# Performance work log

Hardware: AMD Instinct MI355X
Metric: run time of the kernel (lower is better)

Reference implementation:

```python
import jax, jax.numpy as jnp
import numpy as np

B, C, H, W = 64, 2048, 14, 14
D, S, ITERS, EPS, HID = 256, 8, 3, 1e-8, 512


def build_pos(h, w, d):
    gy, gx = np.meshgrid(np.arange(h), np.arange(w), indexing='ij')
    q = d // 4
    omega = 1.0 / (10000.0 ** (np.arange(q) / q))
    ey = gy.reshape(-1, 1) * omega
    ex = gx.reshape(-1, 1) * omega
    pe = np.concatenate([np.sin(ey), np.cos(ey), np.sin(ex), np.cos(ex)], axis=1)
    return jnp.asarray(pe[None], jnp.float32)  # (1, h*w, d)


def layernorm(x, g, b, eps=1e-5):
    m = x.mean(-1, keepdims=True)
    v = ((x - m) ** 2).mean(-1, keepdims=True)
    return (x - m) * jax.lax.rsqrt(v + eps) * g + b


def setup_inputs() -> dict:
    key = jax.random.key(0)
    ks = jax.random.split(key, 16)
    w = lambda k, shp, s=0.02: jax.random.normal(k, shp, jnp.float32) * s
    inp = {
        'x': jax.random.normal(ks[0], (B, C, H, W), jnp.float32),
        'slot_noise': jax.random.normal(ks[1], (B, S, D), jnp.float32),
        'conv_w': w(ks[2], (C, D)), 'conv_b': jnp.zeros((D,), jnp.float32),
        'pos': build_pos(H, W, D),
        'slots_mu': jax.random.normal(ks[3], (1, 1, D), jnp.float32),
        'slots_logsigma': -jnp.ones((1, 1, D), jnp.float32),
        'qw': w(ks[4], (D, D)), 'qb': jnp.zeros((D,), jnp.float32),
        'kw': w(ks[5], (D, D)), 'kb': jnp.zeros((D,), jnp.float32),
        'vw': w(ks[6], (D, D)), 'vb': jnp.zeros((D,), jnp.float32),
        'gru_wih': w(ks[7], (D, 3 * D)), 'gru_whh': w(ks[8], (D, 3 * D)),
        'gru_bih': jnp.zeros((3 * D,), jnp.float32), 'gru_bhh': jnp.zeros((3 * D,), jnp.float32),
        'w1': w(ks[9], (D, HID)), 'b1': jnp.zeros((HID,), jnp.float32),
        'w2': w(ks[10], (HID, D)), 'b2': jnp.zeros((D,), jnp.float32),
        'ln_in_g': jnp.ones((D,), jnp.float32), 'ln_in_b': jnp.zeros((D,), jnp.float32),
        'ln_s_g': jnp.ones((D,), jnp.float32), 'ln_s_b': jnp.zeros((D,), jnp.float32),
        'ln_ff_g': jnp.ones((D,), jnp.float32), 'ln_ff_b': jnp.zeros((D,), jnp.float32),
    }
    return inp


def reference(x, slot_noise, conv_w, conv_b, pos, slots_mu, slots_logsigma,
              qw, qb, kw, kb, vw, vb, gru_wih, gru_whh, gru_bih, gru_bhh,
              w1, b1, w2, b2, ln_in_g, ln_in_b, ln_s_g, ln_s_b, ln_ff_g, ln_ff_b):
    b, c, h, w_ = x.shape
    d = qw.shape[0]
    scale = d ** (-0.5)
    # (B,C,H,W) -> (B,N,C) -> project -> add pos
    xt = x.transpose(0, 2, 3, 1).reshape(b, h * w_, c)
    xt = xt @ conv_w + conv_b + pos
    # slot init
    slots = slots_mu + jnp.exp(slots_logsigma) * slot_noise  # (B,S,D)
    inp = layernorm(xt, ln_in_g, ln_in_b)
    k = inp @ kw + kb
    v = inp @ vw + vb
    attn = None
    for _ in range(ITERS):
        slots_prev = slots
        s = layernorm(slots, ln_s_g, ln_s_b)
        q = s @ qw + qb
        dots = jnp.einsum('bid,bjd->bij', q, k) * scale  # (B,S,N)
        attn = jax.nn.softmax(dots, axis=1) + EPS  # softmax over slots
        attn = attn / attn.sum(-1, keepdims=True)  # renormalize over keys
        updates = jnp.einsum('bjd,bij->bid', v, attn)  # (B,S,D)
        # GRUCell (torch semantics)
        gi = updates @ gru_wih + gru_bih
        gh = slots_prev @ gru_whh + gru_bhh
        ir, iz, inn = jnp.split(gi, 3, axis=-1)
        hr, hz, hn = jnp.split(gh, 3, axis=-1)
        r = jax.nn.sigmoid(ir + hr)
        z = jax.nn.sigmoid(iz + hz)
        nn_ = jnp.tanh(inn + r * hn)
        slots = (1.0 - z) * nn_ + z * slots_prev
        ff = layernorm(slots, ln_ff_g, ln_ff_b)
        slots = slots + (jax.nn.relu(ff @ w1 + b1)) @ w2 + b2
    attn_map = attn.reshape(b, S, h, w_)
    return slots, attn_map
```

## Files before the change

kernel.cpp:

```cpp
#include <hip/hip_runtime.h>
#include <stdint.h>

#define HWN 196
#define CIN 2048
#define DD  256
#define BB  64
#define NSLOT 8
#define KVPAD 224
#define MTOT 12544
#define PPB 208

typedef __attribute__((ext_vector_type(8))) short short8;
typedef __attribute__((ext_vector_type(4))) float f32x4;
typedef __attribute__((ext_vector_type(4))) unsigned short us4;

__device__ __forceinline__ ushort f2bf(float f){ union{float f;uint32_t u;}v;v.f=f;uint32_t u=v.u;return (ushort)((u+0x7FFFu+((u>>16)&1u))>>16);}
__device__ __forceinline__ float bf2f(ushort h){ union{uint32_t u;float f;}v;v.u=((uint32_t)h)<<16;return v.f;}
__device__ __forceinline__ float sigm(float x){ return 1.f/(1.f+expf(-x)); }

__device__ __forceinline__ short8 ldsY(const ushort* buf, int LD, int kt, int lane){
    int row = lane & 15;
    int ch = kt*4 + (lane>>4);
    return *(const short8*)&buf[row*LD + ((ch ^ (row&7))<<3)];
}
__device__ __forceinline__ short8 gX(const ushort* base, int K, int nrow, int kt, int lane){
    return *(const short8*)&base[(size_t)nrow*K + kt*32 + (lane>>4)*8];
}

struct TD { const float* s; ushort* d; int R, C, t0; };
struct TD8 { TD a[8]; };

__global__ __launch_bounds__(256) void k_prep(TD8 td){
    __shared__ float tile[32][33];
    int bt = blockIdx.x;
    int mi = 0;
    #pragma unroll
    for (int i = 1; i < 8; ++i) if (bt >= td.a[i].t0) mi = i;
    TD d = td.a[mi];
    int lt = bt - d.t0;
    int tilesx = (d.C + 31) >> 5;
    int cb = (lt % tilesx) * 32, rb = (lt / tilesx) * 32;
    int tx = threadIdx.x & 31, ty = threadIdx.x >> 5;
    for (int i = ty; i < 32; i += 8) {
        int r = rb + i, c = cb + tx;
        tile[i][tx] = (r < d.R && c < d.C) ? d.s[(size_t)r * d.C + c] : 0.f;
    }
    __syncthreads();
    for (int i = ty; i < 32; i += 8) {
        int c = cb + i, r = rb + tx;
        if (c < d.C && r < d.R) d.d[(size_t)c * d.R + r] = f2bf(tile[tx][i]);
    }
}

__global__ __launch_bounds__(512) void k_proj(const float* __restrict__ x,
        const ushort* __restrict__ cwT, float* __restrict__ Cpart){
    __shared__ ushort As[2][PPB*72];
    const int t = threadIdx.x, lane = t & 63, wv = t >> 6;
    const int bid = blockIdx.x;
    const int b = bid >> 2, nh = (bid >> 1) & 1, kq = bid & 1;
    const int gn = nh*128 + wv*16 + (lane&15);
    const float* xb = x + (size_t)b*(CIN*HWN) + (size_t)(kq*1024)*HWN;
    const ushort* cw = cwT + (size_t)gn*CIN + kq*1024 + (lane>>4)*8;

    f32x4 acc[13] = {};
    f32x4 sreg[7];

    {
        const f32x4* xs = (const f32x4*)xb;
        #pragma unroll
        for (int i = 0; i < 7; ++i){ int idx = t + i*512; if (idx < 3136) sreg[i] = xs[idx]; }
        #pragma unroll
        for (int i = 0; i < 7; ++i){
            int idx = t + i*512;
            if (idx < 3136){
                int c = idx/49, p = (idx - c*49)*4;
                #pragma unroll
                for (int j = 0; j < 4; ++j) As[0][(p+j)*72 + c] = f2bf(sreg[i][j]);
            }
        }
    }
    __syncthreads();
    int cur = 0;
    for (int s = 0; s < 16; ++s){
        if (s < 15){
            const f32x4* xs = (const f32x4*)(xb + (size_t)(s+1)*64*HWN);
            #pragma unroll
            for (int i = 0; i < 7; ++i){ int idx = t + i*512; if (idx < 3136) sreg[i] = xs[idx]; }
        }
        #pragma unroll
        for (int kk = 0; kk < 2; ++kk){
            short8 bf = *(const short8*)&cw[s*64 + kk*32];
            short8 afr[13];
            #pragma unroll
            for (int mi = 0; mi < 13; ++mi)
                afr[mi] = *(const short8*)&As[cur][(mi*16 + (lane&15))*72 + (kk*4 + (lane>>4))*8];
            #pragma unroll
            for (int mi = 0; mi < 13; ++mi)
                acc[mi] = __builtin_amdgcn_mfma_f32_16x16x32_bf16(afr[mi], bf, acc[mi], 0,0,0);
        }
        if (s < 15){
            #pragma unroll
            for (int i = 0; i < 7; ++i){
                int idx = t + i*512;
                if (idx < 3136){
                    int c = idx/49, p = (idx - c*49)*4;
                    #pragma unroll
                    for (int j = 0; j < 4; ++j) As[cur^1][(p+j)*72 + c] = f2bf(sreg[i][j]);
                }
            }
        }
        __syncthreads();
        cur ^= 1;
    }
    float* outp = Cpart + (size_t)kq*MTOT*DD;
    #pragma unroll
    for (int mi = 0; mi < 13; ++mi){
        #pragma unroll
        for (int r = 0; r < 4; ++r){
            int p = mi*16 + (lane>>4)*4 + r;
            if (p < HWN)
                outp[(size_t)(b*HWN + p)*DD + gn] = acc[mi][r];
        }
    }
}

__global__ __launch_bounds__(512) void k_red(const float* __restrict__ Cpart,
        const float* __restrict__ cb, const float* __restrict__ pos,
        const float* __restrict__ lng, const float* __restrict__ lnb,
        const ushort* __restrict__ kwT, const ushort* __restrict__ vwT,
        const float* __restrict__ kb, const float* __restrict__ vb,
        ushort* __restrict__ kbf, ushort* __restrict__ vT){
    __shared__ ushort As[32*256];
    const int t = threadIdx.x, lane = t & 63, wv = t >> 6;
    const int b = blockIdx.x / 7, pblk = blockIdx.x % 7;
    {
        int row = t >> 4, seg = t & 15;
        int pin = pblk*32 + row;
        int grow = b*HWN + pin;
        if (grow > MTOT-1) grow = MTOT-1;
        int p = pin < HWN ? pin : HWN-1;
        const float* c0 = Cpart + (size_t)grow*DD + seg*16;
        const float* c1 = Cpart + (size_t)MTOT*DD + (size_t)grow*DD + seg*16;
        const float* pp = pos + (size_t)p*DD + seg*16;
        float f[16];
        float s = 0.f, sq = 0.f;
        #pragma unroll
        for (int q = 0; q < 4; ++q){
            f32x4 a  = *(const f32x4*)&c0[q*4];
            f32x4 bq = *(const f32x4*)&c1[q*4];
            f32x4 pv = *(const f32x4*)&pp[q*4];
            f32x4 cv = *(const f32x4*)&cb[seg*16 + q*4];
            #pragma unroll
            for (int r2 = 0; r2 < 4; ++r2){
                float v = a[r2] + bq[r2] + pv[r2] + cv[r2];
                f[q*4+r2] = v; s += v; sq += v*v;
            }
        }
        #pragma unroll
        for (int m = 8; m >= 1; m >>= 1){ s += __shfl_xor(s, m, 64); sq += __shfl_xor(sq, m, 64); }
        float mean = s * (1.f/256.f);
        float rs = rsqrtf(sq*(1.f/256.f) - mean*mean + 1e-5f);
        int d0 = seg*16;
        short8 o0, o1;
        #pragma unroll
        for (int j = 0; j < 8; ++j){
            o0[j] = (short)f2bf((f[j]   - mean)*rs*lng[d0+j]   + lnb[d0+j]);
            o1[j] = (short)f2bf((f[8+j] - mean)*rs*lng[d0+8+j] + lnb[d0+8+j]);
        }
        int ch0 = seg*2;
        *(short8*)&As[row*256 + ((ch0^(row&7))<<3)] = o0;
        *(short8*)&As[row*256 + (((ch0+1)^(row&7))<<3)] = o1;
    }
    __syncthreads();
    f32x4 acck[2][2] = {}, accv[2][2] = {};
    const int n0 = wv*32;
    #pragma unroll
    for (int kt = 0; kt < 8; ++kt){
        short8 afr[2];
        #pragma unroll
        for (int mi = 0; mi < 2; ++mi){
            int row = mi*16 + (lane&15);
            int ch = kt*4 + (lane>>4);
            afr[mi] = *(const short8*)&As[row*256 + ((ch^(row&7))<<3)];
        }
        #pragma unroll
        for (int ni = 0; ni < 2; ++ni){
            int n = n0 + ni*16 + (lane&15);
            int koff = kt*32 + (lane>>4)*8;
            short8 bk = *(const short8*)&kwT[(size_t)n*DD + koff];
            short8 bv = *(const short8*)&vwT[(size_t)n*DD + koff];
            #pragma unroll
            for (int mi = 0; mi < 2; ++mi){
                acck[mi][ni] = __builtin_amdgcn_mfma_f32_16x16x32_bf16(afr[mi], bk, acck[mi][ni],0,0,0);
                accv[mi][ni] = __builtin_amdgcn_mfma_f32_16x16x32_bf16(afr[mi], bv, accv[mi][ni],0,0,0);
            }
        }
    }
    #pragma unroll
    for (int mi = 0; mi < 2; ++mi){
        #pragma unroll
        for (int ni = 0; ni < 2; ++ni){
            int n = n0 + ni*16 + (lane&15);
            float kbn = kb[n], vbn = vb[n];
            int pl0 = pblk*32 + mi*16 + (lane>>4)*4;
            us4 pk;
            #pragma unroll
            for (int r = 0; r < 4; ++r){
                kbf[((size_t)b*KVPAD + pl0 + r)*DD + n] = f2bf(acck[mi][ni][r] + kbn);
                pk[r] = f2bf(accv[mi][ni][r] + vbn);
            }
            *(us4*)&vT[((size_t)b*DD + n)*KVPAD + pl0] = pk;
        }
    }
}

__global__ __launch_bounds__(512) void k_init(const float* __restrict__ noise,
        const float* __restrict__ mu, const float* __restrict__ lsig,
        const ushort* __restrict__ qwT, const float* __restrict__ qb,
        const float* __restrict__ gs, const float* __restrict__ bs,
        float* __restrict__ slots, ushort* __restrict__ qbuf){
    __shared__ float Sld[16*256];
    __shared__ ushort Ysn[16*256];
    __shared__ float part[8][16][2];
    __shared__ float stats[16][2];
    const int t = threadIdx.x, lane = t & 63, w = t >> 6;
    const int bb = blockIdx.x, rbase = bb*16;
    {
        int row = t>>5, ch = t&31; int d = ch*8;
        f32x4 n0 = *(const f32x4*)&noise[(size_t)(rbase+row)*DD + d];
        f32x4 n1 = *(const f32x4*)&noise[(size_t)(rbase+row)*DD + d + 4];
        f32x4 m0 = *(const f32x4*)&mu[d];
        f32x4 m1 = *(const f32x4*)&mu[d+4];
        f32x4 l0 = *(const f32x4*)&lsig[d];
        f32x4 l1 = *(const f32x4*)&lsig[d+4];
        f32x4 s0, s1;
        #pragma unroll
        for (int j = 0; j < 4; ++j){
            s0[j] = m0[j] + expf(l0[j])*n0[j];
            s1[j] = m1[j] + expf(l1[j])*n1[j];
        }
        *(f32x4*)&slots[(size_t)(rbase+row)*DD + d] = s0;
        *(f32x4*)&slots[(size_t)(rbase+row)*DD + d + 4] = s1;
        *(f32x4*)&Sld[row*256 + d] = s0;
        *(f32x4*)&Sld[row*256 + d + 4] = s1;
    }
    __syncthreads();
    f32x4 sv[2];
    #pragma unroll
    for (int sub = 0; sub < 2; ++sub){
        int d0 = w*32 + sub*16 + (lane>>4)*4;
        sv[sub] = *(const f32x4*)&Sld[(lane&15)*256 + d0];
    }
    {
        float lsum = 0.f, lsq = 0.f;
        #pragma unroll
        for (int sub = 0; sub < 2; ++sub)
            #pragma unroll
            for (int r = 0; r < 4; ++r){ float v = sv[sub][r]; lsum += v; lsq += v*v; }
        lsum += __shfl_xor(lsum, 16, 64); lsum += __shfl_xor(lsum, 32, 64);
        lsq  += __shfl_xor(lsq, 16, 64);  lsq  += __shfl_xor(lsq, 32, 64);
        if (lane < 16){ part[w][lane][0] = lsum; part[w][lane][1] = lsq; }
    }
    __syncthreads();
    if (t < 16){
        float a = 0.f, c = 0.f;
        #pragma unroll
        for (int i = 0; i < 8; ++i){ a += part[i][t][0]; c += part[i][t][1]; }
        float mean = a*(1.f/256.f);
        stats[t][0] = mean;
        stats[t][1] = rsqrtf(c*(1.f/256.f) - mean*mean + 1e-5f);
    }
    __syncthreads();
    {
        int slot = lane&15;
        float mean = stats[slot][0], rs = stats[slot][1];
        #pragma unroll
        for (int sub = 0; sub < 2; ++sub){
            int d0 = w*32 + sub*16 + (lane>>4)*4;
            f32x4 g4 = *(const f32x4*)&gs[d0];
            f32x4 b4 = *(const f32x4*)&bs[d0];
            us4 o;
            #pragma unroll
            for (int r = 0; r < 4; ++r) o[r] = f2bf((sv[sub][r]-mean)*rs*g4[r] + b4[r]);
            int ch = d0>>3;
            *(us4*)&Ysn[slot*256 + ((ch^(slot&7))<<3) + (d0&7)] = o;
        }
    }
    __syncthreads();
    f32x4 qa[2] = {};
    #pragma unroll
    for (int kt = 0; kt < 8; ++kt){
        short8 ysn = ldsY(Ysn, 256, kt, lane);
        #pragma unroll
        for (int sub = 0; sub < 2; ++sub){
            int nrow = w*32 + sub*16 + (lane&15);
            short8 xx = gX(qwT, 256, nrow, kt, lane);
            qa[sub] = __builtin_amdgcn_mfma_f32_16x16x32_bf16(xx, ysn, qa[sub], 0,0,0);
        }
    }
    #pragma unroll
    for (int sub = 0; sub < 2; ++sub){
        int qd0 = w*32 + sub*16 + (lane>>4)*4;
        f32x4 qb4 = *(const f32x4*)&qb[qd0];
        us4 o;
        #pragma unroll
        for (int r = 0; r < 4; ++r) o[r] = f2bf((qa[sub][r]+qb4[r])*0.0625f);
        *(us4*)&qbuf[(size_t)(rbase+(lane&15))*DD + qd0] = o;
    }
}

__device__ __forceinline__ float sm_ep(f32x4 acc, int f, int lane, ushort* Xat, int srow){
    int k0 = f*16 + (lane>>4)*4;
    us4 o;
    float ps = 0.f;
    #pragma unroll
    for (int r = 0; r < 4; ++r){
        float v = acc[r];
        float mx = v;
        mx = fmaxf(mx, __shfl_xor(mx, 1, 64));
        mx = fmaxf(mx, __shfl_xor(mx, 2, 64));
        mx = fmaxf(mx, __shfl_xor(mx, 4, 64));
        float e = expf(v - mx);
        float se = e;
        se += __shfl_xor(se, 1, 64);
        se += __shfl_xor(se, 2, 64);
        se += __shfl_xor(se, 4, 64);
        float val = e/se + 1e-8f;
        if (k0 + r >= HWN) val = 0.f;
        ps += val;
        o[r] = f2bf(val);
    }
    int ch = k0 >> 3;
    *(us4*)&Xat[srow*256 + ((ch^(srow&7))<<3) + (k0&7)] = o;
    return ps;
}

__global__ __launch_bounds__(512, 2) void k_slot(
        const ushort* __restrict__ qbuf, const ushort* __restrict__ kbf,
        const ushort* __restrict__ vT, float* __restrict__ slots,
        ushort* __restrict__ qout,
        const ushort* __restrict__ wihT, const ushort* __restrict__ whhT,
        const float* __restrict__ bih, const float* __restrict__ bhh,
        const ushort* __restrict__ w1T, const float* __restrict__ b1,
        const ushort* __restrict__ w2T, const float* __restrict__ b2,
        const float* __restrict__ gff, const float* __restrict__ bff,
        const float* __restrict__ gs, const float* __restrict__ bs,
        const ushort* __restrict__ qwT, const float* __restrict__ qb,
        float* __restrict__ out_slots, float* __restrict__ out_attn,
        int final_){
    __shared__ ushort Yq[16*256];
    __shared__ ushort Xat[16*256];
    __shared__ ushort Yupd[16*256];
    __shared__ ushort Yslb[16*256];
    __shared__ ushort Ysn[16*256];
    __shared__ ushort Yh[16*512];
    __shared__ float wpart[8][16];
    __shared__ float invk[16];
    __shared__ float part[8][16][2];
    __shared__ float stats[16][2];
    const int t = threadIdx.x, lane = t & 63, w = t >> 6;
    const int b = blockIdx.x;
    const int rbase = b * NSLOT;
    const int srow = lane & 15;
    const int srd = (srow < NSLOT) ? srow : 0;

    if (t < 256){
        int row = t>>5, ch = t&31;
        short8 v = *(const short8*)&qbuf[(size_t)(rbase+row)*DD + ch*8];
        *(short8*)&Yq[row*256 + ((ch^(row&7))<<3)] = v;
        f32x4 s0 = *(const f32x4*)&slots[(size_t)(rbase+row)*DD + ch*8];
        f32x4 s1 = *(const f32x4*)&slots[(size_t)(rbase+row)*DD + ch*8 + 4];
        short8 sv;
        #pragma unroll
        for (int j = 0; j < 4; ++j){ sv[j] = (short)f2bf(s0[j]); sv[4+j] = (short)f2bf(s1[j]); }
        *(short8*)&Yslb[row*256 + ((ch^(row&7))<<3)] = sv;
    } else {
        int i = t - 256;
        int row = (i>>5) + 8, ch = i&31;
        short8 z;
        #pragma unroll
        for (int j = 0; j < 8; ++j) z[j] = 0;
        *(short8*)&Yq[row*256 + ((ch^(row&7))<<3)] = z;
        *(short8*)&Yupd[row*256 + ((ch^(row&7))<<3)] = z;
        *(short8*)&Yslb[row*256 + ((ch^(row&7))<<3)] = z;
    }
    __syncthreads();
    {
        short8 yf[8];
        #pragma unroll
        for (int kt = 0; kt < 8; ++kt) yf[kt] = ldsY(Yq, 256, kt, lane);
        const ushort* kb_ = kbf + (size_t)b*KVPAD*DD;
        const int f0 = w, f1 = w + 8;
        const bool v1 = (f1 < 14);
        const int r0 = f0*16 + (lane&15), r1 = f1*16 + (lane&15);
        short8 xa[2], xb[2];
        xa[0] = gX(kb_, 256, r0, 0, lane);
        if (v1) xb[0] = gX(kb_, 256, r1, 0, lane);
        f32x4 accA = {}, accB = {};
        #pragma unroll
        for (int kt = 0; kt < 8; ++kt){
            int cu = kt & 1, nx = cu ^ 1;
            if (kt < 7){
                xa[nx] = gX(kb_, 256, r0, kt+1, lane);
                if (v1) xb[nx] = gX(kb_, 256, r1, kt+1, lane);
            }
            accA = __builtin_amdgcn_mfma_f32_16x16x32_bf16(xa[cu], yf[kt], accA, 0,0,0);
            if (v1) accB = __builtin_amdgcn_mfma_f32_16x16x32_bf16(xb[cu], yf[kt], accB, 0,0,0);
        }
        float ps = sm_ep(accA, f0, lane, Xat, srow);
        if (v1) ps += sm_ep(accB, f1, lane, Xat, srow);
        ps += __shfl_xor(ps, 16, 64);
        ps += __shfl_xor(ps, 32, 64);
        if (lane < 16) wpart[w][lane] = ps;
    }
    __syncthreads();
    if (t < 16){
        float s = 0.f;
        #pragma unroll
        for (int i = 0; i < 8; ++i) s += wpart[i][t];
        invk[t] = 1.f/s;
    }
    f32x4 pvacc[2];
    {
        short8 xat[7];
        #pragma unroll
        for (int kt = 0; kt < 7; ++kt) xat[kt] = ldsY(Xat, 256, kt, lane);
        const ushort* vb_ = vT + (size_t)b*DD*KVPAD;
        const int d0a = (w*2)*16 + (lane&15), d0b = (w*2+1)*16 + (lane&15);
        short8 ya[2], yb[2];
        ya[0] = gX(vb_, KVPAD, d0a, 0, lane);
        yb[0] = gX(vb_, KVPAD, d0b, 0, lane);
        f32x4 aA = {}, aB = {};
        #pragma unroll
        for (int kt = 0; kt < 7; ++kt){
            int cu = kt & 1, nx = cu ^ 1;
            if (kt < 6){
                ya[nx] = gX(vb_, KVPAD, d0a, kt+1, lane);
                yb[nx] = gX(vb_, KVPAD, d0b, kt+1, lane);
            }
            aA = __builtin_amdgcn_mfma_f32_16x16x32_bf16(xat[kt], ya[cu], aA, 0,0,0);
            aB = __builtin_amdgcn_mfma_f32_16x16x32_bf16(xat[kt], yb[cu], aB, 0,0,0);
        }
        pvacc[0] = aA; pvacc[1] = aB;
    }
    __syncthreads();
    {
        f32x4 iv = *(const f32x4*)&invk[(lane>>4)*4];
        #pragma unroll
        for (int i = 0; i < 2; ++i){
            int d0 = (w*2 + i)*16;
            #pragma unroll
            for (int r = 0; r < 4; ++r){
                int s2 = (lane>>4)*4 + r;
                if (s2 < NSLOT){
                    int d = d0 + (lane&15);
                    int ch = d >> 3;
                    Yupd[s2*256 + ((ch^(s2&7))<<3) + (d&7)] = f2bf(pvacc[i][r]*iv[r]);
                }
            }
        }
    }
    if (final_){
        for (int idx = t; idx < NSLOT*HWN; idx += 512){
            int slot = idx/HWN, key = idx - slot*HWN;
            int ch = key >> 3;
            out_attn[(size_t)b*NSLOT*HWN + idx] =
                bf2f(Xat[slot*256 + ((ch^(slot&7))<<3) + (key&7)]) * invk[slot];
        }
    }
    __syncthreads();
    f32x4 gi[6] = {}, gh[6] = {};
    {
        int nrw[6];
        #pragma unroll
        for (int g = 0; g < 3; ++g)
            #pragma unroll
            for (int sub = 0; sub < 2; ++sub)
                nrw[g*2+sub] = g*256 + w*32 + sub*16 + (lane&15);
        short8 xw[2][12];
        #pragma unroll
        for (int j = 0; j < 6; ++j){
            xw[0][j]   = gX(wihT, 256, nrw[j], 0, lane);
            xw[0][6+j] = gX(whhT, 256, nrw[j], 0, lane);
        }
        #pragma unroll
        for (int kt = 0; kt < 8; ++kt){
            int cu = kt & 1, nx = cu ^ 1;
            if (kt < 7){
                #pragma unroll
                for (int j = 0; j < 6; ++j){
                    xw[nx][j]   = gX(wihT, 256, nrw[j], kt+1, lane);
                    xw[nx][6+j] = gX(whhT, 256, nrw[j], kt+1, lane);
                }
            }
            short8 yu = ldsY(Yupd, 256, kt, lane);
            short8 ys = ldsY(Yslb, 256, kt, lane);
            #pragma unroll
            for (int j = 0; j < 6; ++j){
                gi[j] = __builtin_amdgcn_mfma_f32_16x16x32_bf16(xw[cu][j],   yu, gi[j], 0,0,0);
                gh[j] = __builtin_amdgcn_mfma_f32_16x16x32_bf16(xw[cu][6+j], ys, gh[j], 0,0,0);
            }
        }
    }
    f32x4 snew[2];
    #pragma unroll
    for (int sub = 0; sub < 2; ++sub){
        int d0 = w*32 + sub*16 + (lane>>4)*4;
        f32x4 sp  = *(const f32x4*)&slots[(size_t)(rbase + srd)*DD + d0];
        f32x4 bir = *(const f32x4*)&bih[d0];
        f32x4 biz = *(const f32x4*)&bih[256 + d0];
        f32x4 bin = *(const f32x4*)&bih[512 + d0];
        f32x4 bhr = *(const f32x4*)&bhh[d0];
        f32x4 bhz = *(const f32x4*)&bhh[256 + d0];
        f32x4 bhn = *(const f32x4*)&bhh[512 + d0];
        #pragma unroll
        for (int r = 0; r < 4; ++r){
            float ir = gi[0+sub][r] + bir[r];
            float iz = gi[2+sub][r] + biz[r];
            float in_ = gi[4+sub][r] + bin[r];
            float hr = gh[0+sub][r] + bhr[r];
            float hz = gh[2+sub][r] + bhz[r];
            float hn = gh[4+sub][r] + bhn[r];
            float rr = sigm(ir + hr);
            float zz = sigm(iz + hz);
            float nn = tanhf(in_ + rr*hn);
            snew[sub][r] = (1.f - zz)*nn + zz*sp[r];
        }
    }
    {
        float lsum = 0.f, lsq = 0.f;
        #pragma unroll
        for (int sub = 0; sub < 2; ++sub)
            #pragma unroll
            for (int r = 0; r < 4; ++r){ float v = snew[sub][r]; lsum += v; lsq += v*v; }
        lsum += __shfl_xor(lsum, 16, 64); lsum += __shfl_xor(lsum, 32, 64);
        lsq  += __shfl_xor(lsq, 16, 64);  lsq  += __shfl_xor(lsq, 32, 64);
        if (lane < 16){ part[w][lane][0] = lsum; part[w][lane][1] = lsq; }
    }
    __syncthreads();
    if (t < 16){
        float a = 0.f, c = 0.f;
        #pragma unroll
        for (int i = 0; i < 8; ++i){ a += part[i][t][0]; c += part[i][t][1]; }
        float mean = a*(1.f/256.f);
        stats[t][0] = mean;
        stats[t][1] = rsqrtf(c*(1.f/256.f) - mean*mean + 1e-5f);
    }
    __syncthreads();
    {
        float mean = stats[srow][0], rs = stats[srow][1];
        #pragma unroll
        for (int sub = 0; sub < 2; ++sub){
            int d0 = w*32 + sub*16 + (lane>>4)*4;
            f32x4 g4 = *(const f32x4*)&gff[d0];
            f32x4 b4 = *(const f32x4*)&bff[d0];
            us4 o;
            #pragma unroll
            for (int r = 0; r < 4; ++r) o[r] = f2bf((snew[sub][r]-mean)*rs*g4[r] + b4[r]);
            int ch = d0 >> 3;
            *(us4*)&Ysn[srow*256 + ((ch^(srow&7))<<3) + (d0&7)] = o;
        }
    }
    __syncthreads();
    {
        int nr1[4];
        #pragma unroll
        for (int s2 = 0; s2 < 4; ++s2) nr1[s2] = w*64 + s2*16 + (lane&15);
        short8 xw1[2][4];
        #pragma unroll
        for (int s2 = 0; s2 < 4; ++s2) xw1[0][s2] = gX(w1T, 256, nr1[s2], 0, lane);
        f32x4 hh[4] = {};
        #pragma unroll
        for (int kt = 0; kt < 8; ++kt){
            int cu = kt & 1, nx = cu ^ 1;
            if (kt < 7){
                #pragma unroll
                for (int s2 = 0; s2 < 4; ++s2) xw1[nx][s2] = gX(w1T, 256, nr1[s2], kt+1, lane);
            }
            short8 ysn = ldsY(Ysn, 256, kt, lane);
            #pragma unroll
            for (int s2 = 0; s2 < 4; ++s2)
                hh[s2] = __builtin_amdgcn_mfma_f32_16x16x32_bf16(xw1[cu][s2], ysn, hh[s2], 0,0,0);
        }
        #pragma unroll
        for (int s2 = 0; s2 < 4; ++s2){
            int n0 = w*64 + s2*16 + (lane>>4)*4;
            f32x4 b14 = *(const f32x4*)&b1[n0];
            us4 o;
            #pragma unroll
            for (int r = 0; r < 4; ++r) o[r] = f2bf(fmaxf(hh[s2][r] + b14[r], 0.f));
            int ch = n0 >> 3;
            *(us4*)&Yh[srow*512 + ((ch^(srow&7))<<3) + (n0&7)] = o;
        }
    }
    __syncthreads();
    f32x4 ns[2];
    {
        int nr2[2];
        #pragma unroll
        for (int sub = 0; sub < 2; ++sub) nr2[sub] = w*32 + sub*16 + (lane&15);
        short8 xw2[2][2];
        #pragma unroll
        for (int sub = 0; sub < 2; ++sub) xw2[0][sub] = gX(w2T, 512, nr2[sub], 0, lane);
        f32x4 o2[2] = {};
        #pragma unroll
        for (int kt = 0; kt < 16; ++kt){
            int cu = kt & 1, nx = cu ^ 1;
            if (kt < 15){
                #pragma unroll
                for (int sub = 0; sub < 2; ++sub) xw2[nx][sub] = gX(w2T, 512, nr2[sub], kt+1, lane);
            }
            short8 yh = ldsY(Yh, 512, kt, lane);
            #pragma unroll
            for (int sub = 0; sub < 2; ++sub)
                o2[sub] = __builtin_amdgcn_mfma_f32_16x16x32_bf16(xw2[cu][sub], yh, o2[sub], 0,0,0);
        }
        float* dst = final_ ? out_slots : slots;
        #pragma unroll
        for (int sub = 0; sub < 2; ++sub){
            int d0 = w*32 + sub*16 + (lane>>4)*4;
            f32x4 b24 = *(const f32x4*)&b2[d0];
            #pragma unroll
            for (int r = 0; r < 4; ++r) ns[sub][r] = o2[sub][r] + b24[r] + snew[sub][r];
            if (srow < NSLOT)
                *(f32x4*)&dst[(size_t)(rbase + srow)*DD + d0] = ns[sub];
        }
    }
    if (final_) return;
    {
        float lsum = 0.f, lsq = 0.f;
        #pragma unroll
        for (int sub = 0; sub < 2; ++sub)
            #pragma unroll
            for (int r = 0; r < 4; ++r){ float v = ns[sub][r]; lsum += v; lsq += v*v; }
        lsum += __shfl_xor(lsum, 16, 64); lsum += __shfl_xor(lsum, 32, 64);
        lsq  += __shfl_xor(lsq, 16, 64);  lsq  += __shfl_xor(lsq, 32, 64);
        if (lane < 16){ part[w][lane][0] = lsum; part[w][lane][1] = lsq; }
    }
    __syncthreads();
    if (t < 16){
        float a = 0.f, c = 0.f;
        #pragma unroll
        for (int i = 0; i < 8; ++i){ a += part[i][t][0]; c += part[i][t][1]; }
        float mean = a*(1.f/256.f);
        stats[t][0] = mean;
        stats[t][1] = rsqrtf(c*(1.f/256.f) - mean*mean + 1e-5f);
    }
    __syncthreads();
    {
        float mean = stats[srow][0], rs = stats[srow][1];
        #pragma unroll
        for (int sub = 0; sub < 2; ++sub){
            int d0 = w*32 + sub*16 + (lane>>4)*4;
            f32x4 g4 = *(const f32x4*)&gs[d0];
            f32x4 b4 = *(const f32x4*)&bs[d0];
            us4 o;
            #pragma unroll
            for (int r = 0; r < 4; ++r) o[r] = f2bf((ns[sub][r]-mean)*rs*g4[r] + b4[r]);
            int ch = d0 >> 3;
            *(us4*)&Ysn[srow*256 + ((ch^(srow&7))<<3) + (d0&7)] = o;
        }
    }
    __syncthreads();
    {
        int nrq[2];
        #pragma unroll
        for (int sub = 0; sub < 2; ++sub) nrq[sub] = w*32 + sub*16 + (lane&15);
        short8 xq[2][2];
        #pragma unroll
        for (int sub = 0; sub < 2; ++sub) xq[0][sub] = gX(qwT, 256, nrq[sub], 0, lane);
        f32x4 qa[2] = {};
        #pragma unroll
        for (int kt = 0; kt < 8; ++kt){
            int cu = kt & 1, nx = cu ^ 1;
            if (kt < 7){
                #pragma unroll
                for (int sub = 0; sub < 2; ++sub) xq[nx][sub] = gX(qwT, 256, nrq[sub], kt+1, lane);
            }
            short8 ysn = ldsY(Ysn, 256, kt, lane);
            #pragma unroll
            for (int sub = 0; sub < 2; ++sub)
                qa[sub] = __builtin_amdgcn_mfma_f32_16x16x32_bf16(xq[cu][sub], ysn, qa[sub], 0,0,0);
        }
        #pragma unroll
        for (int sub = 0; sub < 2; ++sub){
            int qd0 = w*32 + sub*16 + (lane>>4)*4;
            f32x4 qb4 = *(const f32x4*)&qb[qd0];
            us4 o;
            #pragma unroll
            for (int r = 0; r < 4; ++r) o[r] = f2bf((qa[sub][r]+qb4[r])*0.0625f);
            if (srow < NSLOT)
                *(us4*)&qout[(size_t)(rbase + srow)*DD + qd0] = o;
        }
    }
}

extern "C" void kernel_launch(void* const* d_in, const int* in_sizes, int n_in,
                              void* d_out, int out_size, void* d_ws, size_t ws_size,
                              hipStream_t stream) {
    const float* x      = (const float*)d_in[0];
    const float* noise  = (const float*)d_in[1];
    const float* conv_w = (const float*)d_in[2];
    const float* conv_b = (const float*)d_in[3];
    const float* pos    = (const float*)d_in[4];
    const float* mu     = (const float*)d_in[5];
    const float* logsig = (const float*)d_in[6];
    const float* qw  = (const float*)d_in[7];
    const float* qb  = (const float*)d_in[8];
    const float* kw  = (const float*)d_in[9];
    const float* kb  = (const float*)d_in[10];
    const float* vw  = (const float*)d_in[11];
    const float* vb  = (const float*)d_in[12];
    const float* wih = (const float*)d_in[13];
    const float* whh = (const float*)d_in[14];
    const float* bih = (const float*)d_in[15];
    const float* bhh = (const float*)d_in[16];
    const float* w1  = (const float*)d_in[17];
    const float* b1  = (const float*)d_in[18];
    const float* w2  = (const float*)d_in[19];
    const float* b2  = (const float*)d_in[20];
    const float* g_in = (const float*)d_in[21];
    const float* b_in = (const float*)d_in[22];
    const float* g_s  = (const float*)d_in[23];
    const float* b_s  = (const float*)d_in[24];
    const float* g_ff = (const float*)d_in[25];
    const float* b_ff = (const float*)d_in[26];

    char* w = (char*)d_ws;
    ushort* kbf    = (ushort*)w; w += (size_t)BB*KVPAD*DD*2;
    ushort* vT     = (ushort*)w; w += (size_t)BB*DD*KVPAD*2;
    ushort* cwT    = (ushort*)w; w += (size_t)DD*CIN*2;
    ushort* qwT    = (ushort*)w; w += (size_t)DD*DD*2;
    ushort* kwT    = (ushort*)w; w += (size_t)DD*DD*2;
    ushort* vwT    = (ushort*)w; w += (size_t)DD*DD*2;
    ushort* wihT   = (ushort*)w; w += (size_t)768*DD*2;
    ushort* whhT   = (ushort*)w; w += (size_t)768*DD*2;
    ushort* w1T    = (ushort*)w; w += (size_t)512*DD*2;
    ushort* w2T    = (ushort*)w; w += (size_t)DD*512*2;
    ushort* qbb    = (ushort*)w; w += (size_t)BB*NSLOT*DD*2;
    float*  slotsb = (float*)w;  w += (size_t)BB*NSLOT*DD*4;
    float*  Cpart  = (float*)w;  w += (size_t)2*MTOT*DD*4;

    float* out_slots = (float*)d_out;
    float* out_attn  = (float*)d_out + (size_t)BB*NSLOT*DD;

    TD8 td;
    td.a[0] = { conv_w, cwT, 2048, 256,    0 };
    td.a[1] = { qw,     qwT,  256, 256,  512 };
    td.a[2] = { kw,     kwT,  256, 256,  576 };
    td.a[3] = { vw,     vwT,  256, 256,  640 };
    td.a[4] = { wih,    wihT, 256, 768,  704 };
    td.a[5] = { whh,    whhT, 256, 768,  896 };
    td.a[6] = { w1,     w1T,  256, 512, 1088 };
    td.a[7] = { w2,     w2T,  512, 256, 1216 };

    k_prep<<<1344, 256, 0, stream>>>(td);
    k_proj<<<256, 512, 0, stream>>>(x, cwT, Cpart);
    k_red<<<448, 512, 0, stream>>>(Cpart, conv_b, pos, g_in, b_in,
                                   kwT, vwT, kb, vb, kbf, vT);
    k_init<<<32, 512, 0, stream>>>(noise, mu, logsig, qwT, qb, g_s, b_s, slotsb, qbb);
    for (int it = 0; it < 3; ++it){
        k_slot<<<BB, 512, 0, stream>>>(qbb, kbf, vT, slotsb, qbb,
                                       wihT, whhT, bih, bhh, w1T, b1, w2T, b2,
                                       g_ff, b_ff, g_s, b_s, qwT, qb,
                                       out_slots, out_attn, it == 2);
    }
}
```

Measured before the change: 266.9 us.

## Retile input projection GEMM and fuse bias/pos epilogue with bf16 output

Replaces the split-K projection kernel, which wrote two fp32 partial buffers, with a conventional 64x128 tiled GEMM over the flattened (B*HW) rows. Bias and positional encoding are added in the epilogue, and the result is stored once as bf16. The follow-on kernel now only reads bf16 rows before layernorm and the K/V projection. This removes the fp32 partial writes and the reduction traffic. In exchange, the new A loads are strided scalar global reads with no double buffering, and the intermediate loses precision by being rounded to bf16 before layernorm.

```diff
diff --git a/kernel.cpp b/kernel.cpp
--- a/kernel.cpp
+++ b/kernel.cpp
@@ -8,7 +8,6 @@
 #define NSLOT 8
 #define KVPAD 224
 #define MTOT 12544
-#define PPB 208
 
 typedef __attribute__((ext_vector_type(8))) short short8;
 typedef __attribute__((ext_vector_type(4))) float f32x4;
@@ -52,110 +51,109 @@
     }
 }
 
-__global__ __launch_bounds__(512) void k_proj(const float* __restrict__ x,
-        const ushort* __restrict__ cwT, float* __restrict__ Cpart){
-    __shared__ ushort As[2][PPB*72];
-    const int t = threadIdx.x, lane = t & 63, wv = t >> 6;
-    const int bid = blockIdx.x;
-    const int b = bid >> 2, nh = (bid >> 1) & 1, kq = bid & 1;
-    const int gn = nh*128 + wv*16 + (lane&15);
-    const float* xb = x + (size_t)b*(CIN*HWN) + (size_t)(kq*1024)*HWN;
-    const ushort* cw = cwT + (size_t)gn*CIN + kq*1024 + (lane>>4)*8;
-
-    f32x4 acc[13] = {};
-    f32x4 sreg[7];
-
-    {
-        const f32x4* xs = (const f32x4*)xb;
-        #pragma unroll
-        for (int i = 0; i < 7; ++i){ int idx = t + i*512; if (idx < 3136) sreg[i] = xs[idx]; }
-        #pragma unroll
-        for (int i = 0; i < 7; ++i){
-            int idx = t + i*512;
-            if (idx < 3136){
-                int c = idx/49, p = (idx - c*49)*4;
+__global__ __launch_bounds__(256) void k_proj(const float* __restrict__ x,
+        const ushort* __restrict__ bT, const float* __restrict__ cb,
+        const float* __restrict__ pos, ushort* __restrict__ xt){
+    __shared__ ushort As[64 * 64];
+    __shared__ ushort Bs[128 * 64];
+    const int t = threadIdx.x;
+    const int lane = t & 63;
+    const int wv = t >> 6;
+    const int wm = wv >> 1, wn = wv & 1;
+    const int bm = blockIdx.x * 64;
+    const int bn = blockIdx.y * 128;
+
+    const int am = t & 63;
+    const int mg = bm + am;
+    const int ab = mg / HWN, ap = mg % HWN;
+    const float* aptr = x + (size_t)ab * (CIN * HWN) + ap;
+    const int achb = t >> 6;
+
+    const int bnl = t >> 1;
+    const int bch0 = (t & 1) * 4;
+    const ushort* bptr = bT + (size_t)(bn + bnl) * CIN;
+
+    f32x4 acc[2][4] = {};
+
+    for (int k0 = 0; k0 < CIN; k0 += 64) {
+        if (k0) __syncthreads();
+        #pragma unroll
+        for (int p = 0; p < 2; ++p) {
+            int ch = achb + 4 * p;
+            short8 av;
+            #pragma unroll
+            for (int j = 0; j < 8; ++j)
+                av[j] = (short)f2bf(aptr[(size_t)(k0 + ch * 8 + j) * HWN]);
+            *(short8*)&As[am * 64 + ((ch ^ (am & 7)) << 3)] = av;
+        }
+        #pragma unroll
+        for (int c = 0; c < 4; ++c) {
+            int ch = bch0 + c;
+            short8 bv = *(const short8*)&bptr[k0 + ch * 8];
+            *(short8*)&Bs[bnl * 64 + ((ch ^ (bnl & 7)) << 3)] = bv;
+        }
+        __syncthreads();
+        #pragma unroll
+        for (int kk = 0; kk < 2; ++kk) {
+            short8 afr[2], bfr[4];
+            #pragma unroll
+            for (int mi = 0; mi < 2; ++mi) {
+                int row = wm * 32 + mi * 16 + (lane & 15);
+                int ch = kk * 4 + (lane >> 4);
+                afr[mi] = *(const short8*)&As[row * 64 + ((ch ^ (row & 7)) << 3)];
+            }
+            #pragma unroll
+            for (int ni = 0; ni < 4; ++ni) {
+                int row = wn * 64 + ni * 16 + (lane & 15);
+                int ch = kk * 4 + (lane >> 4);
+                bfr[ni] = *(const short8*)&Bs[row * 64 + ((ch ^ (row & 7)) << 3)];
+            }
+            #pragma unroll
+            for (int mi = 0; mi < 2; ++mi)
                 #pragma unroll
-                for (int j = 0; j < 4; ++j) As[0][(p+j)*72 + c] = f2bf(sreg[i][j]);
-            }
-        }
-    }
-    __syncthreads();
-    int cur = 0;
-    for (int s = 0; s < 16; ++s){
-        if (s < 15){
-            const f32x4* xs = (const f32x4*)(xb + (size_t)(s+1)*64*HWN);
-            #pragma unroll
-            for (int i = 0; i < 7; ++i){ int idx = t + i*512; if (idx < 3136) sreg[i] = xs[idx]; }
-        }
-        #pragma unroll
-        for (int kk = 0; kk < 2; ++kk){
-            short8 bf = *(const short8*)&cw[s*64 + kk*32];
-            short8 afr[13];
-            #pragma unroll
-            for (int mi = 0; mi < 13; ++mi)
-                afr[mi] = *(const short8*)&As[cur][(mi*16 + (lane&15))*72 + (kk*4 + (lane>>4))*8];
-            #pragma unroll
-            for (int mi = 0; mi < 13; ++mi)
-                acc[mi] = __builtin_amdgcn_mfma_f32_16x16x32_bf16(afr[mi], bf, acc[mi], 0,0,0);
-        }
-        if (s < 15){
-            #pragma unroll
-            for (int i = 0; i < 7; ++i){
-                int idx = t + i*512;
-                if (idx < 3136){
-                    int c = idx/49, p = (idx - c*49)*4;
-                    #pragma unroll
-                    for (int j = 0; j < 4; ++j) As[cur^1][(p+j)*72 + c] = f2bf(sreg[i][j]);
-                }
-            }
-        }
-        __syncthreads();
-        cur ^= 1;
-    }
-    float* outp = Cpart + (size_t)kq*MTOT*DD;
-    #pragma unroll
-    for (int mi = 0; mi < 13; ++mi){
-        #pragma unroll
-        for (int r = 0; r < 4; ++r){
-            int p = mi*16 + (lane>>4)*4 + r;
-            if (p < HWN)
-                outp[(size_t)(b*HWN + p)*DD + gn] = acc[mi][r];
-        }
-    }
-}
-
-__global__ __launch_bounds__(512) void k_red(const float* __restrict__ Cpart,
-        const float* __restrict__ cb, const float* __restrict__ pos,
-        const float* __restrict__ lng, const float* __restrict__ lnb,
+                for (int ni = 0; ni < 4; ++ni)
+                    acc[mi][ni] = __builtin_amdgcn_mfma_f32_16x16x32_bf16(
+                        afr[mi], bfr[ni], acc[mi][ni], 0, 0, 0);
+        }
+    }
+    #pragma unroll
+    for (int mi = 0; mi < 2; ++mi) {
+        #pragma unroll
+        for (int ni = 0; ni < 4; ++ni) {
+            int n = bn + wn * 64 + ni * 16 + (lane & 15);
+            float cbn = cb[n];
+            #pragma unroll
+            for (int r = 0; r < 4; ++r) {
+                int row = wm * 32 + mi * 16 + (lane >> 4) * 4 + r;
+                int m = bm + row;
+                int p = m % HWN;
+                xt[(size_t)m * DD + n] = f2bf(acc[mi][ni][r] + cbn + pos[(size_t)p * DD + n]);
+            }
+        }
+    }
+}
+
+__global__ __launch_bounds__(512) void k_kv(const ushort* __restrict__ xt,
         const ushort* __restrict__ kwT, const ushort* __restrict__ vwT,
         const float* __restrict__ kb, const float* __restrict__ vb,
+        const float* __restrict__ lng, const float* __restrict__ lnb,
         ushort* __restrict__ kbf, ushort* __restrict__ vT){
     __shared__ ushort As[32*256];
     const int t = threadIdx.x, lane = t & 63, wv = t >> 6;
     const int b = blockIdx.x / 7, pblk = blockIdx.x % 7;
     {
         int row = t >> 4, seg = t & 15;
-        int pin = pblk*32 + row;
-        int grow = b*HWN + pin;
+        int grow = b*HWN + pblk*32 + row;
         if (grow > MTOT-1) grow = MTOT-1;
-        int p = pin < HWN ? pin : HWN-1;
-        const float* c0 = Cpart + (size_t)grow*DD + seg*16;
-        const float* c1 = Cpart + (size_t)MTOT*DD + (size_t)grow*DD + seg*16;
-        const float* pp = pos + (size_t)p*DD + seg*16;
+        const ushort* src = &xt[(size_t)grow*DD + seg*16];
+        short8 v0 = *(const short8*)&src[0];
+        short8 v1 = *(const short8*)&src[8];
         float f[16];
+        #pragma unroll
+        for (int j = 0; j < 8; ++j){ f[j] = bf2f((ushort)v0[j]); f[8+j] = bf2f((ushort)v1[j]); }
         float s = 0.f, sq = 0.f;
         #pragma unroll
-        for (int q = 0; q < 4; ++q){
-            f32x4 a  = *(const f32x4*)&c0[q*4];
-            f32x4 bq = *(const f32x4*)&c1[q*4];
-            f32x4 pv = *(const f32x4*)&pp[q*4];
-            f32x4 cv = *(const f32x4*)&cb[seg*16 + q*4];
-            #pragma unroll
-            for (int r2 = 0; r2 < 4; ++r2){
-                float v = a[r2] + bq[r2] + pv[r2] + cv[r2];
-                f[q*4+r2] = v; s += v; sq += v*v;
-            }
-        }
+        for (int j = 0; j < 16; ++j){ s += f[j]; sq += f[j]*f[j]; }
         #pragma unroll
         for (int m = 8; m >= 1; m >>= 1){ s += __shfl_xor(s, m, 64); sq += __shfl_xor(sq, m, 64); }
         float mean = s * (1.f/256.f);
@@ -739,7 +737,7 @@
     ushort* w2T    = (ushort*)w; w += (size_t)DD*512*2;
     ushort* qbb    = (ushort*)w; w += (size_t)BB*NSLOT*DD*2;
     float*  slotsb = (float*)w;  w += (size_t)BB*NSLOT*DD*4;
-    float*  Cpart  = (float*)w;  w += (size_t)2*MTOT*DD*4;
+    ushort* xt     = (ushort*)w; w += (size_t)MTOT*DD*2;
 
     float* out_slots = (float*)d_out;
     float* out_attn  = (float*)d_out + (size_t)BB*NSLOT*DD;
@@ -755,9 +753,8 @@
     td.a[7] = { w2,     w2T,  512, 256, 1216 };
 
     k_prep<<<1344, 256, 0, stream>>>(td);
-    k_proj<<<256, 512, 0, stream>>>(x, cwT, Cpart);
-    k_red<<<448, 512, 0, stream>>>(Cpart, conv_b, pos, g_in, b_in,
-                                   kwT, vwT, kb, vb, kbf, vT);
+    k_proj<<<dim3(196, 2), 256, 0, stream>>>(x, cwT, conv_b, pos, xt);
+    k_kv<<<448, 512, 0, stream>>>(xt, kwT, vwT, kb, vb, g_in, b_in, kbf, vT);
     k_init<<<32, 512, 0, stream>>>(noise, mu, logsig, qwT, qb, g_s, b_s, slotsb, qbb);
     for (int it = 0; it < 3; ++it){
         k_slot<<<BB, 512, 0, stream>>>(qbb, kbf, vT, slotsb, qbb,
```

Result: faster. 238.3 us (-10.7%).
